# Optimization experiments

Hardware: AMD Instinct MI355X
Metric: run time of the kernel (lower is better)

The kernel has to match this reference:

```python
import jax, jax.numpy as jnp
import numpy as np

T, A = 10, 9           # input_dim_h, input_dim_w
HID = 128              # EncoderMLP hidden_dim default
D = 512                # n_latent_dims
G, K = 4, 32           # vqvae_groups, vqvae_n_embed
ACT_SCALE = 1.0


def setup_inputs() -> dict:
    key = jax.random.key(0)
    ks = jax.random.split(key, 16)
    N = 131072
    s = lambda k, shp, fan: jax.random.normal(k, shp, jnp.float32) * (1.0 / np.sqrt(fan))
    inp = {
        "state": jax.random.normal(ks[0], (N, T, A), jnp.float32),
        # encoder: (T*A)->128 relu, 128->128 relu, 128->512
        "enc_w1": s(ks[1], (T * A, HID), T * A), "enc_b1": jnp.zeros((HID,), jnp.float32),
        "enc_w2": s(ks[2], (HID, HID), HID),     "enc_b2": jnp.zeros((HID,), jnp.float32),
        "enc_w3": s(ks[3], (HID, D), HID),       "enc_b3": jnp.zeros((D,), jnp.float32),
        # decoder: 512->128 relu, 128->128 relu, 128->(T*A)
        "dec_w1": s(ks[4], (D, HID), D),         "dec_b1": jnp.zeros((HID,), jnp.float32),
        "dec_w2": s(ks[5], (HID, HID), HID),     "dec_b2": jnp.zeros((HID,), jnp.float32),
        "dec_w3": s(ks[6], (HID, T * A), HID),   "dec_b3": jnp.zeros((T * A,), jnp.float32),
        # residual VQ codebooks [G, K, D]
        "codebooks": jax.random.normal(ks[7], (G, K, D), jnp.float32),
    }
    return inp


def _mlp(x, w1, b1, w2, b2, w3, b3):
    h = jax.nn.relu(x @ w1 + b1)
    h = jax.nn.relu(h @ w2 + b2)
    return h @ w3 + b3


def reference(state, enc_w1, enc_b1, enc_w2, enc_b2, enc_w3, enc_b3,
              dec_w1, dec_b1, dec_w2, dec_b2, dec_w3, dec_b3, codebooks):
    N = state.shape[0]
    x = (state / ACT_SCALE).reshape(N, T * A)            # preprocess: 'N T A -> N (T A)'
    z = _mlp(x, enc_w1, enc_b1, enc_w2, enc_b2, enc_w3, enc_b3)  # [N, D]

    # Residual VQ over G quantizers (eval path): nearest-code per residual,
    # straight-through accumulation, per-quantizer commitment loss.
    residual = z
    quant = jnp.zeros_like(z)
    codes, losses = [], []
    for g in range(G):
        e = codebooks[g]                                  # [K, D]
        # ||r - e||^2 = ||r||^2 - 2 r.e + ||e||^2 ; ||r||^2 constant over K
        dist = jnp.sum(e * e, axis=-1)[None, :] - 2.0 * (residual @ e.T)  # [N, K]
        idx = jnp.argmin(dist, axis=-1)                   # [N]
        q = e[idx]                                        # [N, D] gather
        losses.append(jnp.mean((jax.lax.stop_gradient(q) - residual) ** 2))
        quant = quant + residual + jax.lax.stop_gradient(q - residual)  # straight-through
        residual = residual - jax.lax.stop_gradient(q)
        codes.append(idx)
    vq_code = jnp.stack(codes, axis=-1)                   # [N, G]
    vq_loss = jnp.sum(jnp.stack(losses))

    recon = _mlp(quant, dec_w1, dec_b1, dec_w2, dec_b2, dec_w3, dec_b3) * ACT_SCALE
    recon = recon.reshape(N, T, A)                        # 'N (T A) -> N T A'
    return quant, vq_code, recon, vq_loss
```

## Files before the change

### kernel.cpp

```cpp
#include <hip/hip_runtime.h>
#include <hip/hip_bf16.h>

#define NSAMP 131072
#define TA    90
#define HID   128
#define DLAT  512

#define OFF_CODE  67108864ll
#define OFF_RECON (67108864ll + 524288ll)
#define OFF_LOSS  (67108864ll + 524288ll + 11796480ll)

#define PZF    8704
#define SHF    8960
#define MSKF   8256
#define H2AF   8272
#define H2BF   8400
#define TAU    0.08f

typedef __attribute__((ext_vector_type(8))) short bf16x8;
typedef __attribute__((ext_vector_type(4))) short s16x4;
typedef __attribute__((ext_vector_type(4))) float f32x4;
typedef unsigned short ushort_t;
#define MFMA16(a, b, c) __builtin_amdgcn_mfma_f32_16x16x32_bf16(a, b, c, 0, 0, 0)

__device__ __forceinline__ ushort_t f2bf(float f) {
    unsigned u = __float_as_uint(f);
    u = (u + 0x7FFF + ((u >> 16) & 1)) >> 16;
    return (ushort_t)u;
}
__device__ __forceinline__ float bf2f(ushort_t u) {
    return __uint_as_float(((unsigned)u) << 16);
}
__device__ __forceinline__ void nt_store4(float* p, float x0, float x1,
                                          float x2, float x3) {
    f32x4 v = {x0, x1, x2, x3};
    __builtin_nontemporal_store(v, (f32x4*)p);
}

__device__ __forceinline__ float dot512(const float* __restrict__ a,
                                        const float* __restrict__ b) {
    float s = 0.f;
    for (int i = 0; i < 128; ++i) {
        float4 x = ((const float4*)a)[i], y = ((const float4*)b)[i];
        s += x.x * y.x + x.y * y.y + x.z * y.z + x.w * y.w;
    }
    return s;
}

__global__ void k_prep(const float* __restrict__ cb, const float* __restrict__ w3,
                       const float* __restrict__ b3, const float* __restrict__ w1d,
                       const float* __restrict__ w2d, const float* __restrict__ w3d,
                       const float* __restrict__ w2e, const float* __restrict__ w1e,
                       float* __restrict__ P, float* __restrict__ M,
                       float* __restrict__ t0, float* __restrict__ v,
                       float* __restrict__ csc, float* __restrict__ cbW,
                       ushort_t* __restrict__ Qbf, ushort_t* __restrict__ w2bf,
                       ushort_t* __restrict__ w3bf,
                       ushort_t* __restrict__ Mhibf, ushort_t* __restrict__ Mlobf,
                       ushort_t* __restrict__ w2ehi, ushort_t* __restrict__ w2elo,
                       ushort_t* __restrict__ w1ehi, ushort_t* __restrict__ w1elo) {
    int tbl = blockIdx.x >> 6;
    int gid = (blockIdx.x & 63) * 256 + threadIdx.x;
    int i = gid >> 7, j = gid & 127;
    if (tbl == 0) {
        P[gid] = dot512(cb + (size_t)i * 512, cb + (size_t)j * 512);
        if (gid < 128) t0[gid] = dot512(cb + (size_t)gid * 512, b3);
        if (gid == 0) csc[0] = dot512(b3, b3);
    } else if (tbl == 1) {
        M[gid] = dot512(w3 + (size_t)i * 512, cb + (size_t)j * 512);
    } else if (tbl == 2) {
        Qbf[gid] = f2bf(dot512(w3 + (size_t)i * 512, w3 + (size_t)j * 512));
        if (gid < 128) v[gid] = dot512(w3 + (size_t)gid * 512, b3);
    } else if (tbl == 3) {
        float s = 0.f;
        for (int d = 0; d < 512; ++d) s = fmaf(cb[(size_t)i * 512 + d], w1d[d * 128 + j], s);
        cbW[gid] = s;
    } else if (tbl == 4) {
        w2bf[gid] = f2bf(w2d[j * 128 + i]);
    } else if (tbl == 5) {
        if (gid < 96 * 128)
            w3bf[gid] = (i < 90) ? f2bf(w3d[j * TA + i]) : (ushort_t)0;
    } else if (tbl == 6) {
        float d = dot512(w3 + (size_t)j * 512, cb + (size_t)i * 512);
        ushort_t hi = f2bf(d);
        Mhibf[gid] = hi;
        Mlobf[gid] = f2bf(d - bf2f(hi));
    } else if (tbl == 7) {
        float d = w2e[j * 128 + i];
        ushort_t hi = f2bf(d);
        w2ehi[gid] = hi;
        w2elo[gid] = f2bf(d - bf2f(hi));
    } else {
        float d = (j < 90) ? w1e[(size_t)j * 128 + i] : 0.f;
        ushort_t hi = f2bf(d);
        w1ehi[gid] = hi;
        w1elo[gid] = f2bf(d - bf2f(hi));
    }
}

__device__ __forceinline__ void enc_body(
        const float* __restrict__ X,
        const float* __restrict__ ew1, const float* __restrict__ eb1,
        const float* __restrict__ ew2, const float* __restrict__ eb2,
        const ushort_t* __restrict__ w1ehi, const ushort_t* __restrict__ w1elo,
        const ushort_t* __restrict__ w2ehi, const ushort_t* __restrict__ w2elo,
        const float* __restrict__ Mt, const ushort_t* __restrict__ Qbf,
        const ushort_t* __restrict__ Mhi, const ushort_t* __restrict__ Mlo,
        const float* __restrict__ t0g, const float* __restrict__ vg,
        const float* __restrict__ cg, const float* __restrict__ Pg,
        float* __restrict__ codes_out, float* __restrict__ loss_acc,
        float* SH, int t, int row0, int (&cs)[4]) {
    ushort_t* sphi = (ushort_t*)SH;
    ushort_t* splo = (ushort_t*)(SH + 4096);
    const int wv = t >> 6, lane = t & 63, lr = lane & 15, lg = lane >> 4;

    for (int it = 0; it < 24; ++it) {
        int idx = it * 256 + t;
        int s = idx / 96, j = idx - 96 * s;
        float xv = (j < 90) ? X[(size_t)(row0 + s) * TA + j] : 0.f;
        ushort_t hi = f2bf(xv);
        int adr = ((s << 7) + j) ^ ((s & 7) << 3);
        sphi[adr] = hi;
        splo[adr] = f2bf(xv - bf2f(hi));
    }
    __syncthreads();

    {
        f32x4 c1[2][4];
#pragma unroll
        for (int m = 0; m < 2; ++m)
#pragma unroll
            for (int n = 0; n < 4; ++n) c1[m][n] = (f32x4){0.f, 0.f, 0.f, 0.f};
#pragma unroll
        for (int kt = 0; kt < 3; ++kt) {
            bf16x8 ah[2], al[2], bhi[4], blo[4];
#pragma unroll
            for (int m = 0; m < 2; ++m) {
                int arow = (32 * wv + 16 * m + lr) * 128 + kt * 32 + lg * 8;
                ah[m] = *(const bf16x8*)&w1ehi[arow];
                al[m] = *(const bf16x8*)&w1elo[arow];
            }
#pragma unroll
            for (int n = 0; n < 4; ++n) {
                int s = 16 * n + lr;
                int adr = ((s << 7) + kt * 32 + lg * 8) ^ ((s & 7) << 3);
                bhi[n] = *(const bf16x8*)&sphi[adr];
                blo[n] = *(const bf16x8*)&splo[adr];
            }
#pragma unroll
            for (int m = 0; m < 2; ++m)
#pragma unroll
                for (int n = 0; n < 4; ++n) {
                    c1[m][n] = MFMA16(ah[m], bhi[n], c1[m][n]);
                    c1[m][n] = MFMA16(ah[m], blo[n], c1[m][n]);
                    c1[m][n] = MFMA16(al[m], bhi[n], c1[m][n]);
                }
        }
        __syncthreads();
        float rbf[2][4];
#pragma unroll
        for (int m = 0; m < 2; ++m)
#pragma unroll
            for (int r = 0; r < 4; ++r) rbf[m][r] = eb1[32 * wv + 16 * m + lg * 4 + r];
#pragma unroll
        for (int m = 0; m < 2; ++m)
#pragma unroll
            for (int n = 0; n < 4; ++n) {
                int s = 16 * n + lr;
                s16x4 ph, pl;
#pragma unroll
                for (int r = 0; r < 4; ++r) {
                    float hv = fmaxf(c1[m][n][r] + rbf[m][r], 0.f);
                    ushort_t hi = f2bf(hv);
                    ph[r] = (short)hi;
                    pl[r] = (short)f2bf(hv - bf2f(hi));
                }
                int ob2 = 32 * wv + 16 * m + lg * 4;
                int adr = ((s << 7) + ob2) ^ ((s & 7) << 3);
                *(s16x4*)&sphi[adr] = ph;
                *(s16x4*)&splo[adr] = pl;
            }
    }
    __syncthreads();

    {
        f32x4 c2[2][4];
#pragma unroll
        for (int m = 0; m < 2; ++m)
#pragma unroll
            for (int n = 0; n < 4; ++n) c2[m][n] = (f32x4){0.f, 0.f, 0.f, 0.f};
#pragma unroll
        for (int kt = 0; kt < 4; ++kt) {
            bf16x8 ah[2], al[2], bhi[4], blo[4];
#pragma unroll
            for (int m = 0; m < 2; ++m) {
                int arow = (32 * wv + 16 * m + lr) * 128 + kt * 32 + lg * 8;
                ah[m] = *(const bf16x8*)&w2ehi[arow];
                al[m] = *(const bf16x8*)&w2elo[arow];
            }
#pragma unroll
            for (int n = 0; n < 4; ++n) {
                int s = 16 * n + lr;
                int adr = ((s << 7) + kt * 32 + lg * 8) ^ ((s & 7) << 3);
                bhi[n] = *(const bf16x8*)&sphi[adr];
                blo[n] = *(const bf16x8*)&splo[adr];
            }
#pragma unroll
            for (int m = 0; m < 2; ++m)
#pragma unroll
                for (int n = 0; n < 4; ++n) {
                    c2[m][n] = MFMA16(ah[m], bhi[n], c2[m][n]);
                    c2[m][n] = MFMA16(ah[m], blo[n], c2[m][n]);
                    c2[m][n] = MFMA16(al[m], bhi[n], c2[m][n]);
                }
        }
        __syncthreads();
        float rbf[2][4];
#pragma unroll
        for (int m = 0; m < 2; ++m)
#pragma unroll
            for (int r = 0; r < 4; ++r) rbf[m][r] = eb2[32 * wv + 16 * m + lg * 4 + r];
#pragma unroll
        for (int m = 0; m < 2; ++m)
#pragma unroll
            for (int n = 0; n < 4; ++n) {
                int s = 16 * n + lr;
                s16x4 ph, pl;
#pragma unroll
                for (int r = 0; r < 4; ++r) {
                    float hv = fmaxf(c2[m][n][r] + rbf[m][r], 0.f);
                    ushort_t hi = f2bf(hv);
                    ph[r] = (short)hi;
                    pl[r] = (short)f2bf(hv - bf2f(hi));
                }
                int ob2 = 32 * wv + 16 * m + lg * 4;
                int adr = ((s << 7) + ob2) ^ ((s & 7) << 3);
                *(s16x4*)&sphi[adr] = ph;
                *(s16x4*)&splo[adr] = pl;
            }
    }
    __syncthreads();

    f32x4 sc[2][4];
    {
        f32x4 qc[2][4];
#pragma unroll
        for (int m = 0; m < 2; ++m)
#pragma unroll
            for (int n = 0; n < 4; ++n) {
                qc[m][n] = (f32x4){0.f, 0.f, 0.f, 0.f};
                sc[m][n] = (f32x4){0.f, 0.f, 0.f, 0.f};
            }
#pragma unroll
        for (int kt = 0; kt < 4; ++kt) {
            bf16x8 aq[2], amh[2], aml[2], bhi[4], blo[4];
#pragma unroll
            for (int m = 0; m < 2; ++m) {
                int arow = (32 * wv + 16 * m + lr) * 128 + kt * 32 + lg * 8;
                aq[m]  = *(const bf16x8*)&Qbf[arow];
                amh[m] = *(const bf16x8*)&Mhi[arow];
                aml[m] = *(const bf16x8*)&Mlo[arow];
            }
#pragma unroll
            for (int n = 0; n < 4; ++n) {
                int s = 16 * n + lr;
                int adr = ((s << 7) + kt * 32 + lg * 8) ^ ((s & 7) << 3);
                bhi[n] = *(const bf16x8*)&sphi[adr];
                blo[n] = *(const bf16x8*)&splo[adr];
            }
#pragma unroll
            for (int m = 0; m < 2; ++m)
#pragma unroll
                for (int n = 0; n < 4; ++n) {
                    qc[m][n] = MFMA16(aq[m], bhi[n], qc[m][n]);
                    sc[m][n] = MFMA16(amh[m], bhi[n], sc[m][n]);
                    sc[m][n] = MFMA16(amh[m], blo[n], sc[m][n]);
                    sc[m][n] = MFMA16(aml[m], bhi[n], sc[m][n]);
                }
        }
        float v2[2][4];
#pragma unroll
        for (int m = 0; m < 2; ++m)
#pragma unroll
            for (int r = 0; r < 4; ++r) v2[m][r] = 2.f * vg[32 * wv + 16 * m + lg * 4 + r];
#pragma unroll
        for (int n = 0; n < 4; ++n) {
            int s = 16 * n + lr;
            float p = 0.f;
#pragma unroll
            for (int m = 0; m < 2; ++m)
#pragma unroll
                for (int r = 0; r < 4; ++r) {
                    int o = 32 * wv + 16 * m + lg * 4 + r;
                    int adr = ((s << 7) + o) ^ ((s & 7) << 3);
                    float hv = bf2f(sphi[adr]) + bf2f(splo[adr]);
                    p = fmaf(qc[m][n][r] + v2[m][r], hv, p);
                }
            p += __shfl_xor(p, 16);
            p += __shfl_xor(p, 32);
            if (lg == 0) SH[PZF + wv * 64 + s] = p;
        }
    }
    __syncthreads();

#pragma unroll
    for (int m = 0; m < 2; ++m)
#pragma unroll
        for (int n = 0; n < 4; ++n) {
            int s = 16 * n + lr;
#pragma unroll
            for (int r = 0; r < 4; ++r) {
                int o = 32 * wv + 16 * m + lg * 4 + r;
                SH[s * 129 + o] = sc[m][n][r] + t0g[o];
            }
        }
    __syncthreads();

    if (t < 64) {
        float marg = 3.4e38f;
#pragma unroll
        for (int g = 0; g < 4; ++g) {
            float best = 3.4e38f, best2 = 3.4e38f; int bi = g * 32;
#pragma unroll
            for (int k = 0; k < 32; ++k) {
                int c = g * 32 + k;
                float zd = SH[t * 129 + c];
                float nr = Pg[c * 128 + c];
                float a2 = 0.f;
#pragma unroll
                for (int gp = 0; gp < g; ++gp) a2 += Pg[cs[gp] * 128 + c];
                float dist = nr - 2.f * (zd - a2);
                if (dist < best) { best2 = best; best = dist; bi = c; }
                else if (dist < best2) { best2 = dist; }
            }
            cs[g] = bi;
            float m2 = best2 - best;
            marg = (m2 < marg) ? m2 : marg;
        }
        unsigned long long mk = __ballot(marg < TAU);
        if (t == 0) *(unsigned long long*)&SH[MSKF] = mk;
    }
    __syncthreads();

    const unsigned long long mask = *(const unsigned long long*)&SH[MSKF];

    {
        unsigned long long mk = mask;
        while (mk) {
            int nA = (int)__ffsll((long long)mk) - 1; mk &= mk - 1;
            int nB = -1;
            if (mk) { nB = (int)__ffsll((long long)mk) - 1; mk &= mk - 1; }
            int grp = t >> 7, tt = t & 127;
            int s2 = grp ? nB : nA;
            float hv1 = 0.f;
            if (s2 >= 0) {
                const float* xr = X + (size_t)(row0 + s2) * TA;
                for (int j = 0; j < 90; ++j)
                    hv1 = fmaf(xr[j], ew1[j * 128 + tt], hv1);
                hv1 = fmaxf(hv1 + eb1[tt], 0.f);
                SH[(grp ? H2BF : H2AF) + tt] = hv1;
            }
            __syncthreads();
            float hv2 = 0.f;
            if (s2 >= 0) {
                const float* h1c = &SH[grp ? H2BF : H2AF];
                for (int j = 0; j < 128; ++j)
                    hv2 = fmaf(h1c[j], ew2[(size_t)j * 128 + tt], hv2);
                hv2 = fmaxf(hv2 + eb2[tt], 0.f);
            }
            __syncthreads();
            if (s2 >= 0) SH[(grp ? H2BF : H2AF) + tt] = hv2;
            __syncthreads();
            if (s2 >= 0) {
                const float* h2c = &SH[grp ? H2BF : H2AF];
                float a = 0.f;
                for (int j = 0; j < 128; ++j)
                    a = fmaf(h2c[j], Mt[(size_t)j * 128 + tt], a);
                SH[s2 * 129 + tt] = a + t0g[tt];
            }
            __syncthreads();
        }
    }

    if (t < 64 && ((mask >> t) & 1ull)) {
#pragma unroll
        for (int g = 0; g < 4; ++g) {
            float best = 3.4e38f; int bi = g * 32;
#pragma unroll
            for (int k = 0; k < 32; ++k) {
                int c = g * 32 + k;
                float zd = SH[t * 129 + c];
                float nr = Pg[c * 128 + c];
                float a2 = 0.f;
#pragma unroll
                for (int gp = 0; gp < g; ++gp) a2 += Pg[cs[gp] * 128 + c];
                float dist = nr - 2.f * (zd - a2);
                if (dist < best) { best = dist; bi = c; }
            }
            cs[g] = bi;
        }
    }

    if (t < 64) {
        float znorm = cg[0] + SH[PZF + t] + SH[PZF + 64 + t]
                    + SH[PZF + 128 + t] + SH[PZF + 192 + t];
        float S1 = 0.f, Sp = 0.f, msum = 0.f;
#pragma unroll
        for (int g = 0; g < 4; ++g) {
            int c = cs[g];
            float zd = SH[t * 129 + c];
            float nr = Pg[c * 128 + c];
            float a2 = 0.f;
#pragma unroll
            for (int gp = 0; gp < g; ++gp) a2 += Pg[cs[gp] * 128 + c];
            S1 += zd;
            Sp += nr + 2.f * a2;
            msum += (znorm - 2.f * S1 + Sp);
            codes_out[(size_t)(row0 + t) * 4 + g] = (float)(cs[g] - g * 32);
        }
#pragma unroll
        for (int off = 32; off; off >>= 1) msum += __shfl_down(msum, off);
        if (t == 0) atomicAdd(&loss_acc[0], msum);
    }
}

__device__ __forceinline__ void dec_body(
        const float* __restrict__ cb, const float* __restrict__ cbW,
        const float* __restrict__ b1, const ushort_t* __restrict__ w2bf,
        const float* __restrict__ b2, const ushort_t* __restrict__ w3bf,
        const float* __restrict__ b3,
        float* __restrict__ quant_out, float* __restrict__ recon_out,
        unsigned char* SHB, int t, int row0) {
    int* cods = (int*)SHB;
    ushort_t* h2bf = (ushort_t*)SHB;
    ushort_t* h1bf = (ushort_t*)(SHB + 16384);
    float* Rl = (float*)(SHB + 16384);
    const int st = t & 15, ct = t >> 4;
    const int s0 = st * 4, o0 = ct * 8;

    float rb1[8];
#pragma unroll
    for (int i = 0; i < 8; ++i) rb1[i] = b1[o0 + i];

    for (int i = 0; i < 32; ++i) {
        int idx4 = i * 256 + t;
        int s = idx4 >> 7, d4 = (idx4 & 127) * 4;
        const int* cp = &cods[s * 4];
        float4 a = *(const float4*)&cb[(size_t)cp[0] * 512 + d4];
        float4 b = *(const float4*)&cb[(size_t)cp[1] * 512 + d4];
        float4 c = *(const float4*)&cb[(size_t)cp[2] * 512 + d4];
        float4 d = *(const float4*)&cb[(size_t)cp[3] * 512 + d4];
        nt_store4(&quant_out[(size_t)(row0 + s) * 512 + d4],
                  a.x + b.x + c.x + d.x, a.y + b.y + c.y + d.y,
                  a.z + b.z + c.z + d.z, a.w + b.w + c.w + d.w);
    }

    {
        float accL[8][4];
#pragma unroll
        for (int b = 0; b < 4; ++b) {
            const int* cp = &cods[(s0 + b) * 4];
            float u[8] = {0, 0, 0, 0, 0, 0, 0, 0};
#pragma unroll
            for (int g = 0; g < 4; ++g) {
                const float* r = &cbW[(size_t)cp[g] * 128 + o0];
                float4 x0 = *(const float4*)r, x1 = *(const float4*)(r + 4);
                u[0] += x0.x; u[1] += x0.y; u[2] += x0.z; u[3] += x0.w;
                u[4] += x1.x; u[5] += x1.y; u[6] += x1.z; u[7] += x1.w;
            }
#pragma unroll
            for (int a = 0; a < 8; ++a) accL[a][b] = u[a];
        }
#pragma unroll
        for (int b = 0; b < 4; ++b) {
            int s = s0 + b;
            bf16x8 pk;
#pragma unroll
            for (int a = 0; a < 8; ++a)
                pk[a] = (short)f2bf(fmaxf(accL[a][b] + rb1[a], 0.f));
            *(bf16x8*)&h1bf[((s << 7) + o0) ^ ((s & 7) << 3)] = pk;
        }
    }
    __syncthreads();

    const int wv = t >> 6, lane = t & 63, lr = lane & 15, lg = lane >> 4;

    {
        f32x4 c2[2][4];
#pragma unroll
        for (int m = 0; m < 2; ++m)
#pragma unroll
            for (int n = 0; n < 4; ++n) c2[m][n] = (f32x4){0.f, 0.f, 0.f, 0.f};
#pragma unroll
        for (int kt = 0; kt < 4; ++kt) {
            bf16x8 af[2], bfr[4];
#pragma unroll
            for (int m = 0; m < 2; ++m)
                af[m] = *(const bf16x8*)&w2bf[(32 * wv + 16 * m + lr) * 128 + kt * 32 + lg * 8];
#pragma unroll
            for (int n = 0; n < 4; ++n) {
                int s = 16 * n + lr;
                bfr[n] = *(const bf16x8*)&h1bf[((s << 7) + kt * 32 + lg * 8) ^ ((s & 7) << 3)];
            }
#pragma unroll
            for (int m = 0; m < 2; ++m)
#pragma unroll
                for (int n = 0; n < 4; ++n)
                    c2[m][n] = MFMA16(af[m], bfr[n], c2[m][n]);
        }
        float rb[2][4];
#pragma unroll
        for (int m = 0; m < 2; ++m)
#pragma unroll
            for (int r = 0; r < 4; ++r) rb[m][r] = b2[32 * wv + 16 * m + lg * 4 + r];
#pragma unroll
        for (int m = 0; m < 2; ++m)
#pragma unroll
            for (int n = 0; n < 4; ++n) {
                int s = 16 * n + lr;
                s16x4 pk;
#pragma unroll
                for (int r = 0; r < 4; ++r)
                    pk[r] = (short)f2bf(fmaxf(c2[m][n][r] + rb[m][r], 0.f));
                int ob2 = 32 * wv + 16 * m + lg * 4;
                *(s16x4*)&h2bf[((s << 7) + ob2) ^ ((s & 7) << 3)] = pk;
            }
    }
    __syncthreads();

    {
        f32x4 c3[6];
#pragma unroll
        for (int m = 0; m < 6; ++m) c3[m] = (f32x4){0.f, 0.f, 0.f, 0.f};
        const int sB = 16 * wv + lr;
#pragma unroll
        for (int kt = 0; kt < 4; ++kt) {
            bf16x8 bfr = *(const bf16x8*)&h2bf[((sB << 7) + kt * 32 + lg * 8) ^ ((sB & 7) << 3)];
#pragma unroll
            for (int mt = 0; mt < 6; ++mt) {
                bf16x8 af = *(const bf16x8*)&w3bf[(16 * mt + lr) * 128 + kt * 32 + lg * 8];
                c3[mt] = MFMA16(af, bfr, c3[mt]);
            }
        }
#pragma unroll
        for (int mt = 0; mt < 6; ++mt)
#pragma unroll
            for (int r = 0; r < 4; ++r) {
                int o = 16 * mt + lg * 4 + r;
                if (o < 90) Rl[sB * 90 + o] = c3[mt][r] + b3[o];
            }
    }
    __syncthreads();

    {
        const float4* R4v = (const float4*)Rl;
        float* G = recon_out + (size_t)row0 * 90;
#pragma unroll
        for (int it = 0; it < 6; ++it) {
            int i4 = it * 256 + t;
            if (i4 < 1440) {
                float4 vv = R4v[i4];
                nt_store4(&G[i4 * 4], vv.x, vv.y, vv.z, vv.w);
            }
        }
    }
}

__launch_bounds__(256, 4)
__global__ void k_fused(const float* __restrict__ X,
                        const float* __restrict__ ew1, const float* __restrict__ eb1,
                        const float* __restrict__ ew2, const float* __restrict__ eb2,
                        const ushort_t* __restrict__ w1ehi, const ushort_t* __restrict__ w1elo,
                        const ushort_t* __restrict__ w2ehi, const ushort_t* __restrict__ w2elo,
                        const float* __restrict__ Mt, const ushort_t* __restrict__ Qbf,
                        const ushort_t* __restrict__ Mhi, const ushort_t* __restrict__ Mlo,
                        const float* __restrict__ t0g, const float* __restrict__ vg,
                        const float* __restrict__ cg, const float* __restrict__ Pg,
                        float* __restrict__ codes_out, float* __restrict__ loss_acc,
                        const float* __restrict__ cb, const float* __restrict__ cbW,
                        const float* __restrict__ db1, const ushort_t* __restrict__ w2bf,
                        const float* __restrict__ db2, const ushort_t* __restrict__ w3bf,
                        const float* __restrict__ db3,
                        float* __restrict__ quant_out, float* __restrict__ recon_out) {
    __shared__ __align__(16) unsigned char SHB[39424];
    float* SH = (float*)SHB;
    const int t = threadIdx.x;
    const int row0 = blockIdx.x * 64;

    int cs[4] = {0, 32, 64, 96};
    enc_body(X, ew1, eb1, ew2, eb2, w1ehi, w1elo, w2ehi, w2elo,
             Mt, Qbf, Mhi, Mlo, t0g, vg, cg, Pg, codes_out, loss_acc,
             SH, t, row0, cs);

    __syncthreads();
    if (t < 64) {
#pragma unroll
        for (int g = 0; g < 4; ++g) ((int*)SHB)[t * 4 + g] = cs[g];
    }
    __syncthreads();

    dec_body(cb, cbW, db1, w2bf, db2, w3bf, db3, quant_out, recon_out,
             SHB, t, row0);
}

__launch_bounds__(256, 4)
__global__ void k_encvq(const float* __restrict__ X,
                        const float* __restrict__ w1, const float* __restrict__ b1,
                        const float* __restrict__ w2, const float* __restrict__ b2,
                        const ushort_t* __restrict__ w1ehi, const ushort_t* __restrict__ w1elo,
                        const ushort_t* __restrict__ w2ehi, const ushort_t* __restrict__ w2elo,
                        const float* __restrict__ Mt, const ushort_t* __restrict__ Qbf,
                        const ushort_t* __restrict__ Mhi, const ushort_t* __restrict__ Mlo,
                        const float* __restrict__ t0g, const float* __restrict__ vg,
                        const float* __restrict__ cg, const float* __restrict__ Pg,
                        float* __restrict__ codes_out, float* __restrict__ loss_acc) {
    __shared__ __align__(16) float SH[SHF];
    const int t = threadIdx.x;
    const int row0 = blockIdx.x * 64;
    int cs[4] = {0, 32, 64, 96};
    enc_body(X, w1, b1, w2, b2, w1ehi, w1elo, w2ehi, w2elo,
             Mt, Qbf, Mhi, Mlo, t0g, vg, cg, Pg, codes_out, loss_acc,
             SH, t, row0, cs);
}

__launch_bounds__(256, 4)
__global__ void k_dec(const float* __restrict__ codes_f, const float* __restrict__ cb,
                      const float* __restrict__ cbW, const float* __restrict__ b1,
                      const ushort_t* __restrict__ w2bf, const float* __restrict__ b2,
                      const ushort_t* __restrict__ w3bf, const float* __restrict__ b3,
                      float* __restrict__ quant_out, float* __restrict__ recon_out) {
    __shared__ __align__(16) unsigned char SHB[39424];
    const int t = threadIdx.x;
    const int row0 = blockIdx.x * 64;
    ((int*)SHB)[t] = ((t & 3) << 5) + (int)codes_f[(size_t)row0 * 4 + t];
    __syncthreads();
    dec_body(cb, cbW, b1, w2bf, b2, w3bf, b3, quant_out, recon_out,
             SHB, t, row0);
}

__global__ void k_loss(const float* __restrict__ acc, float* __restrict__ out) {
    out[0] = acc[0] * (1.0f / ((float)NSAMP * (float)DLAT));
}

extern "C" void kernel_launch(void* const* d_in, const int* in_sizes, int n_in,
                              void* d_out, int out_size, void* d_ws, size_t ws_size,
                              hipStream_t stream) {
    const float* state  = (const float*)d_in[0];
    const float* enc_w1 = (const float*)d_in[1];
    const float* enc_b1 = (const float*)d_in[2];
    const float* enc_w2 = (const float*)d_in[3];
    const float* enc_b2 = (const float*)d_in[4];
    const float* enc_w3 = (const float*)d_in[5];
    const float* enc_b3 = (const float*)d_in[6];
    const float* dec_w1 = (const float*)d_in[7];
    const float* dec_b1 = (const float*)d_in[8];
    const float* dec_w2 = (const float*)d_in[9];
    const float* dec_b2 = (const float*)d_in[10];
    const float* dec_w3 = (const float*)d_in[11];
    const float* dec_b3 = (const float*)d_in[12];
    const float* cb     = (const float*)d_in[13];

    float* out = (float*)d_out;
    float* ws = (float*)d_ws;
    float* loss_acc = ws;
    float* cbW = ws + 256;
    ushort_t* Qbf  = (ushort_t*)(ws + 16640);
    ushort_t* w2bf = (ushort_t*)(ws + 24832);
    ushort_t* w3bf = (ushort_t*)(ws + 33024);

    hipMemsetAsync(d_ws, 0, 16, stream);

    const bool big = (ws_size >= (size_t)121728 * 4);
    if (big) {
        float* M   = ws + 39424;
        float* P   = ws + 55808;
        ushort_t* Mhi = (ushort_t*)(ws + 72192);
        ushort_t* Mlo = (ushort_t*)(ws + 80384);
        float* t0  = ws + 88576;
        float* v   = ws + 88704;
        float* csc = ws + 88832;
        ushort_t* w2ehi = (ushort_t*)(ws + 88960);
        ushort_t* w2elo = (ushort_t*)(ws + 97152);
        ushort_t* w1ehi = (ushort_t*)(ws + 105344);
        ushort_t* w1elo = (ushort_t*)(ws + 113536);
        k_prep<<<576, 256, 0, stream>>>(cb, enc_w3, enc_b3, dec_w1, dec_w2, dec_w3,
                                        enc_w2, enc_w1,
                                        P, M, t0, v, csc, cbW, Qbf, w2bf, w3bf,
                                        Mhi, Mlo, w2ehi, w2elo, w1ehi, w1elo);
        k_fused<<<NSAMP / 64, 256, 0, stream>>>(state, enc_w1, enc_b1, enc_w2, enc_b2,
                                                w1ehi, w1elo, w2ehi, w2elo,
                                                M, Qbf, Mhi, Mlo, t0, v, csc, P,
                                                out + OFF_CODE, loss_acc,
                                                cb, cbW, dec_b1, w2bf, dec_b2, w3bf,
                                                dec_b3, out, out + OFF_RECON);
    } else {
        float* P   = out;
        float* M   = out + 16384;
        ushort_t* Mhi = (ushort_t*)(out + 32768);
        ushort_t* Mlo = (ushort_t*)(out + 40960);
        float* t0  = out + 49152;
        float* v   = out + 49280;
        float* csc = out + 49408;
        ushort_t* w2ehi = (ushort_t*)(out + 49664);
        ushort_t* w2elo = (ushort_t*)(out + 57856);
        ushort_t* w1ehi = (ushort_t*)(out + 66048);
        ushort_t* w1elo = (ushort_t*)(out + 74240);
        k_prep<<<576, 256, 0, stream>>>(cb, enc_w3, enc_b3, dec_w1, dec_w2, dec_w3,
                                        enc_w2, enc_w1,
                                        P, M, t0, v, csc, cbW, Qbf, w2bf, w3bf,
                                        Mhi, Mlo, w2ehi, w2elo, w1ehi, w1elo);
        k_encvq<<<NSAMP / 64, 256, 0, stream>>>(state, enc_w1, enc_b1, enc_w2, enc_b2,
                                                w1ehi, w1elo, w2ehi, w2elo,
                                                M, Qbf, Mhi, Mlo, t0, v, csc, P,
                                                out + OFF_CODE, loss_acc);
        k_dec<<<NSAMP / 64, 256, 0, stream>>>(out + OFF_CODE, cb, cbW,
                                              dec_b1, w2bf, dec_b2, w3bf, dec_b3,
                                              out, out + OFF_RECON);
    }
    k_loss<<<1, 1, 0, stream>>>(loss_acc, out + OFF_LOSS);
}
```

Before: 288.6 us.

## Shrink shared memory to raise occupancy and fold znorm into loss accumulator

Drops the per-sample znorm partial buffer and instead accumulates the z·(q+2v) term globally into a second loss accumulator, with the constant term added in the final loss kernel. The z-distance table switches from padded 129-stride to an XOR-swizzled 128-stride layout. Recon staging is split into two halves so the LDS footprint fits in 32 KB. Together these allow launch bounds of 5 blocks per CU. The cost is extra barriers, a global atomic per wave, and a small device copy on the non-fused path.

```diff
diff --git a/kernel.cpp b/kernel.cpp
--- a/kernel.cpp
+++ b/kernel.cpp
@@ -10,12 +10,8 @@
 #define OFF_RECON (67108864ll + 524288ll)
 #define OFF_LOSS  (67108864ll + 524288ll + 11796480ll)
 
-#define PZF    8704
-#define SHF    8960
-#define MSKF   8256
-#define H2AF   8272
-#define H2BF   8400
 #define TAU    0.08f
+#define ZD(s, c) (((s) << 7) + ((c) ^ ((s) & 31)))
 
 typedef __attribute__((ext_vector_type(8))) short bf16x8;
 typedef __attribute__((ext_vector_type(4))) short s16x4;
@@ -107,7 +103,7 @@
         const float* __restrict__ Mt, const ushort_t* __restrict__ Qbf,
         const ushort_t* __restrict__ Mhi, const ushort_t* __restrict__ Mlo,
         const float* __restrict__ t0g, const float* __restrict__ vg,
-        const float* __restrict__ cg, const float* __restrict__ Pg,
+        const float* __restrict__ Pg,
         float* __restrict__ codes_out, float* __restrict__ loss_acc,
         float* SH, int t, int row0, int (&cs)[4]) {
     ushort_t* sphi = (ushort_t*)SH;
@@ -283,10 +279,10 @@
         for (int m = 0; m < 2; ++m)
 #pragma unroll
             for (int r = 0; r < 4; ++r) v2[m][r] = 2.f * vg[32 * wv + 16 * m + lg * 4 + r];
+        float zp = 0.f;
 #pragma unroll
         for (int n = 0; n < 4; ++n) {
             int s = 16 * n + lr;
-            float p = 0.f;
 #pragma unroll
             for (int m = 0; m < 2; ++m)
 #pragma unroll
@@ -294,12 +290,12 @@
                     int o = 32 * wv + 16 * m + lg * 4 + r;
                     int adr = ((s << 7) + o) ^ ((s & 7) << 3);
                     float hv = bf2f(sphi[adr]) + bf2f(splo[adr]);
-                    p = fmaf(qc[m][n][r] + v2[m][r], hv, p);
-                }
-            p += __shfl_xor(p, 16);
-            p += __shfl_xor(p, 32);
-            if (lg == 0) SH[PZF + wv * 64 + s] = p;
-        }
+                    zp = fmaf(qc[m][n][r] + v2[m][r], hv, zp);
+                }
+        }
+#pragma unroll
+        for (int off = 32; off; off >>= 1) zp += __shfl_down(zp, off);
+        if (lane == 0) atomicAdd(&loss_acc[1], zp);
     }
     __syncthreads();
 
@@ -311,12 +307,13 @@
 #pragma unroll
             for (int r = 0; r < 4; ++r) {
                 int o = 32 * wv + 16 * m + lg * 4 + r;
-                SH[s * 129 + o] = sc[m][n][r] + t0g[o];
-            }
-        }
-    __syncthreads();
-
-    if (t < 64) {
+                SH[ZD(s, o)] = sc[m][n][r] + t0g[o];
+            }
+        }
+    __syncthreads();
+
+    unsigned long long mask;
+    {
         float marg = 3.4e38f;
 #pragma unroll
         for (int g = 0; g < 4; ++g) {
@@ -324,7 +321,7 @@
 #pragma unroll
             for (int k = 0; k < 32; ++k) {
                 int c = g * 32 + k;
-                float zd = SH[t * 129 + c];
+                float zd = SH[ZD(lane, c)];
                 float nr = Pg[c * 128 + c];
                 float a2 = 0.f;
 #pragma unroll
@@ -337,12 +334,9 @@
             float m2 = best2 - best;
             marg = (m2 < marg) ? m2 : marg;
         }
-        unsigned long long mk = __ballot(marg < TAU);
-        if (t == 0) *(unsigned long long*)&SH[MSKF] = mk;
-    }
-    __syncthreads();
-
-    const unsigned long long mask = *(const unsigned long long*)&SH[MSKF];
+        mask = __ballot(marg < TAU);
+    }
+    __syncthreads();
 
     {
         unsigned long long mk = mask;
@@ -358,38 +352,39 @@
                 for (int j = 0; j < 90; ++j)
                     hv1 = fmaf(xr[j], ew1[j * 128 + tt], hv1);
                 hv1 = fmaxf(hv1 + eb1[tt], 0.f);
-                SH[(grp ? H2BF : H2AF) + tt] = hv1;
+                SH[(s2 << 7) + tt] = hv1;
             }
             __syncthreads();
             float hv2 = 0.f;
             if (s2 >= 0) {
-                const float* h1c = &SH[grp ? H2BF : H2AF];
+                const float* h1c = &SH[s2 << 7];
                 for (int j = 0; j < 128; ++j)
                     hv2 = fmaf(h1c[j], ew2[(size_t)j * 128 + tt], hv2);
                 hv2 = fmaxf(hv2 + eb2[tt], 0.f);
             }
             __syncthreads();
-            if (s2 >= 0) SH[(grp ? H2BF : H2AF) + tt] = hv2;
+            if (s2 >= 0) SH[(s2 << 7) + tt] = hv2;
             __syncthreads();
+            float a = 0.f;
             if (s2 >= 0) {
-                const float* h2c = &SH[grp ? H2BF : H2AF];
-                float a = 0.f;
+                const float* h2c = &SH[s2 << 7];
                 for (int j = 0; j < 128; ++j)
                     a = fmaf(h2c[j], Mt[(size_t)j * 128 + tt], a);
-                SH[s2 * 129 + tt] = a + t0g[tt];
             }
             __syncthreads();
-        }
-    }
-
-    if (t < 64 && ((mask >> t) & 1ull)) {
+            if (s2 >= 0) SH[ZD(s2, tt)] = a + t0g[tt];
+            __syncthreads();
+        }
+    }
+
+    if ((mask >> lane) & 1ull) {
 #pragma unroll
         for (int g = 0; g < 4; ++g) {
             float best = 3.4e38f; int bi = g * 32;
 #pragma unroll
             for (int k = 0; k < 32; ++k) {
                 int c = g * 32 + k;
-                float zd = SH[t * 129 + c];
+                float zd = SH[ZD(lane, c)];
                 float nr = Pg[c * 128 + c];
                 float a2 = 0.f;
 #pragma unroll
@@ -402,20 +397,18 @@
     }
 
     if (t < 64) {
-        float znorm = cg[0] + SH[PZF + t] + SH[PZF + 64 + t]
-                    + SH[PZF + 128 + t] + SH[PZF + 192 + t];
         float S1 = 0.f, Sp = 0.f, msum = 0.f;
 #pragma unroll
         for (int g = 0; g < 4; ++g) {
             int c = cs[g];
-            float zd = SH[t * 129 + c];
+            float zd = SH[ZD(t, c)];
             float nr = Pg[c * 128 + c];
             float a2 = 0.f;
 #pragma unroll
             for (int gp = 0; gp < g; ++gp) a2 += Pg[cs[gp] * 128 + c];
             S1 += zd;
             Sp += nr + 2.f * a2;
-            msum += (znorm - 2.f * S1 + Sp);
+            msum += (Sp - 2.f * S1);
             codes_out[(size_t)(row0 + t) * 4 + g] = (float)(cs[g] - g * 32);
         }
 #pragma unroll
@@ -542,31 +535,55 @@
                 c3[mt] = MFMA16(af, bfr, c3[mt]);
             }
         }
-#pragma unroll
-        for (int mt = 0; mt < 6; ++mt)
-#pragma unroll
-            for (int r = 0; r < 4; ++r) {
-                int o = 16 * mt + lg * 4 + r;
-                if (o < 90) Rl[sB * 90 + o] = c3[mt][r] + b3[o];
-            }
-    }
-    __syncthreads();
-
-    {
-        const float4* R4v = (const float4*)Rl;
-        float* G = recon_out + (size_t)row0 * 90;
-#pragma unroll
-        for (int it = 0; it < 6; ++it) {
-            int i4 = it * 256 + t;
-            if (i4 < 1440) {
-                float4 vv = R4v[i4];
-                nt_store4(&G[i4 * 4], vv.x, vv.y, vv.z, vv.w);
-            }
-        }
-    }
-}
-
-__launch_bounds__(256, 4)
+        if (sB < 32) {
+#pragma unroll
+            for (int mt = 0; mt < 6; ++mt)
+#pragma unroll
+                for (int r = 0; r < 4; ++r) {
+                    int o = 16 * mt + lg * 4 + r;
+                    if (o < 90) Rl[sB * 90 + o] = c3[mt][r] + b3[o];
+                }
+        }
+        __syncthreads();
+        {
+            const float4* R4v = (const float4*)Rl;
+            float* G = recon_out + (size_t)row0 * 90;
+#pragma unroll
+            for (int it = 0; it < 3; ++it) {
+                int i4 = it * 256 + t;
+                if (i4 < 720) {
+                    float4 vv = R4v[i4];
+                    nt_store4(&G[i4 * 4], vv.x, vv.y, vv.z, vv.w);
+                }
+            }
+        }
+        __syncthreads();
+        if (sB >= 32) {
+#pragma unroll
+            for (int mt = 0; mt < 6; ++mt)
+#pragma unroll
+                for (int r = 0; r < 4; ++r) {
+                    int o = 16 * mt + lg * 4 + r;
+                    if (o < 90) Rl[(sB - 32) * 90 + o] = c3[mt][r] + b3[o];
+                }
+        }
+        __syncthreads();
+        {
+            const float4* R4v = (const float4*)Rl;
+            float* G = recon_out + (size_t)(row0 + 32) * 90;
+#pragma unroll
+            for (int it = 0; it < 3; ++it) {
+                int i4 = it * 256 + t;
+                if (i4 < 720) {
+                    float4 vv = R4v[i4];
+                    nt_store4(&G[i4 * 4], vv.x, vv.y, vv.z, vv.w);
+                }
+            }
+        }
+    }
+}
+
+__launch_bounds__(256, 5)
 __global__ void k_fused(const float* __restrict__ X,
                         const float* __restrict__ ew1, const float* __restrict__ eb1,
                         const float* __restrict__ ew2, const float* __restrict__ eb2,
@@ -575,21 +592,21 @@
                         const float* __restrict__ Mt, const ushort_t* __restrict__ Qbf,
                         const ushort_t* __restrict__ Mhi, const ushort_t* __restrict__ Mlo,
                         const float* __restrict__ t0g, const float* __restrict__ vg,
-                        const float* __restrict__ cg, const float* __restrict__ Pg,
+                        const float* __restrict__ Pg,
                         float* __restrict__ codes_out, float* __restrict__ loss_acc,
                         const float* __restrict__ cb, const float* __restrict__ cbW,
                         const float* __restrict__ db1, const ushort_t* __restrict__ w2bf,
                         const float* __restrict__ db2, const ushort_t* __restrict__ w3bf,
                         const float* __restrict__ db3,
                         float* __restrict__ quant_out, float* __restrict__ recon_out) {
-    __shared__ __align__(16) unsigned char SHB[39424];
+    __shared__ __align__(16) unsigned char SHB[32768];
     float* SH = (float*)SHB;
     const int t = threadIdx.x;
     const int row0 = blockIdx.x * 64;
 
     int cs[4] = {0, 32, 64, 96};
     enc_body(X, ew1, eb1, ew2, eb2, w1ehi, w1elo, w2ehi, w2elo,
-             Mt, Qbf, Mhi, Mlo, t0g, vg, cg, Pg, codes_out, loss_acc,
+             Mt, Qbf, Mhi, Mlo, t0g, vg, Pg, codes_out, loss_acc,
              SH, t, row0, cs);
 
     __syncthreads();
@@ -603,7 +620,7 @@
              SHB, t, row0);
 }
 
-__launch_bounds__(256, 4)
+__launch_bounds__(256, 5)
 __global__ void k_encvq(const float* __restrict__ X,
                         const float* __restrict__ w1, const float* __restrict__ b1,
                         const float* __restrict__ w2, const float* __restrict__ b2,
@@ -612,24 +629,24 @@
                         const float* __restrict__ Mt, const ushort_t* __restrict__ Qbf,
                         const ushort_t* __restrict__ Mhi, const ushort_t* __restrict__ Mlo,
                         const float* __restrict__ t0g, const float* __restrict__ vg,
-                        const float* __restrict__ cg, const float* __restrict__ Pg,
+                        const float* __restrict__ Pg,
                         float* __restrict__ codes_out, float* __restrict__ loss_acc) {
-    __shared__ __align__(16) float SH[SHF];
+    __shared__ __align__(16) float SH[8192];
     const int t = threadIdx.x;
     const int row0 = blockIdx.x * 64;
     int cs[4] = {0, 32, 64, 96};
     enc_body(X, w1, b1, w2, b2, w1ehi, w1elo, w2ehi, w2elo,
-             Mt, Qbf, Mhi, Mlo, t0g, vg, cg, Pg, codes_out, loss_acc,
+             Mt, Qbf, Mhi, Mlo, t0g, vg, Pg, codes_out, loss_acc,
              SH, t, row0, cs);
 }
 
-__launch_bounds__(256, 4)
+__launch_bounds__(256, 5)
 __global__ void k_dec(const float* __restrict__ codes_f, const float* __restrict__ cb,
                       const float* __restrict__ cbW, const float* __restrict__ b1,
                       const ushort_t* __restrict__ w2bf, const float* __restrict__ b2,
                       const ushort_t* __restrict__ w3bf, const float* __restrict__ b3,
                       float* __restrict__ quant_out, float* __restrict__ recon_out) {
-    __shared__ __align__(16) unsigned char SHB[39424];
+    __shared__ __align__(16) unsigned char SHB[32768];
     const int t = threadIdx.x;
     const int row0 = blockIdx.x * 64;
     ((int*)SHB)[t] = ((t & 3) << 5) + (int)codes_f[(size_t)row0 * 4 + t];
@@ -638,8 +655,10 @@
              SHB, t, row0);
 }
 
-__global__ void k_loss(const float* __restrict__ acc, float* __restrict__ out) {
-    out[0] = acc[0] * (1.0f / ((float)NSAMP * (float)DLAT));
+__global__ void k_loss(const float* __restrict__ acc, const float* __restrict__ csc,
+                       float* __restrict__ out) {
+    out[0] = (acc[0] + 4.f * acc[1] + 4.f * (float)NSAMP * csc[0])
+             * (1.0f / ((float)NSAMP * (float)DLAT));
 }
 
 extern "C" void kernel_launch(void* const* d_in, const int* in_sizes, int n_in,
@@ -689,10 +708,11 @@
                                         Mhi, Mlo, w2ehi, w2elo, w1ehi, w1elo);
         k_fused<<<NSAMP / 64, 256, 0, stream>>>(state, enc_w1, enc_b1, enc_w2, enc_b2,
                                                 w1ehi, w1elo, w2ehi, w2elo,
-                                                M, Qbf, Mhi, Mlo, t0, v, csc, P,
+                                                M, Qbf, Mhi, Mlo, t0, v, P,
                                                 out + OFF_CODE, loss_acc,
                                                 cb, cbW, dec_b1, w2bf, dec_b2, w3bf,
                                                 dec_b3, out, out + OFF_RECON);
+        k_loss<<<1, 1, 0, stream>>>(loss_acc, csc, out + OFF_LOSS);
     } else {
         float* P   = out;
         float* M   = out + 16384;
@@ -709,13 +729,14 @@
                                         enc_w2, enc_w1,
                                         P, M, t0, v, csc, cbW, Qbf, w2bf, w3bf,
                                         Mhi, Mlo, w2ehi, w2elo, w1ehi, w1elo);
+        hipMemcpyAsync(ws + 8, csc, 4, hipMemcpyDeviceToDevice, stream);
         k_encvq<<<NSAMP / 64, 256, 0, stream>>>(state, enc_w1, enc_b1, enc_w2, enc_b2,
                                                 w1ehi, w1elo, w2ehi, w2elo,
-                                                M, Qbf, Mhi, Mlo, t0, v, csc, P,
+                                                M, Qbf, Mhi, Mlo, t0, v, P,
                                                 out + OFF_CODE, loss_acc);
         k_dec<<<NSAMP / 64, 256, 0, stream>>>(out + OFF_CODE, cb, cbW,
                                               dec_b1, w2bf, dec_b2, w3bf, dec_b3,
                                               out, out + OFF_RECON);
-    }
-    k_loss<<<1, 1, 0, stream>>>(loss_acc, out + OFF_LOSS);
-}
+        k_loss<<<1, 1, 0, stream>>>(loss_acc, ws + 8, out + OFF_LOSS);
+    }
+}
```

Result: slower. 508.4 us (+76.2%).
